# Kernel optimization log

Measured on AMD Instinct MI355X. Metric: run time of the kernel, lower is better.

## Reference

```python
import jax, jax.numpy as jnp
import numpy as np

EPS = 1e-5

def _layernorm(x, g, b):
    m = jnp.mean(x, axis=-1, keepdims=True)
    v = jnp.mean(jnp.square(x - m), axis=-1, keepdims=True)
    return (x - m) * jax.lax.rsqrt(v + EPS) * g + b

def setup_inputs() -> dict:
    key = jax.random.key(0)
    B, S, D, H = 2, 2048, 1024, 16
    F = 4 * D
    ks = jax.random.split(key, 12)
    s = 1.0 / np.sqrt(D)
    inp = {
        "x": jax.random.normal(ks[0], (B, S, D), dtype=jnp.float32),
        "mask": jnp.ones((B, S), dtype=jnp.int32),
        "wq": jax.random.normal(ks[1], (D, D), dtype=jnp.float32) * s,
        "bq": jnp.zeros((D,), jnp.float32),
        "wk": jax.random.normal(ks[2], (D, D), dtype=jnp.float32) * s,
        "bk": jnp.zeros((D,), jnp.float32),
        "wv": jax.random.normal(ks[3], (D, D), dtype=jnp.float32) * s,
        "bv": jnp.zeros((D,), jnp.float32),
        "wo": jax.random.normal(ks[4], (D, D), dtype=jnp.float32) * s,
        "bo": jnp.zeros((D,), jnp.float32),
        "g1": jnp.ones((D,), jnp.float32),
        "be1": jnp.zeros((D,), jnp.float32),
        "g2": jnp.ones((D,), jnp.float32),
        "be2": jnp.zeros((D,), jnp.float32),
        "w1": jax.random.normal(ks[5], (D, F), dtype=jnp.float32) * s,
        "bf1": jnp.zeros((F,), jnp.float32),
        "w2": jax.random.normal(ks[6], (F, D), dtype=jnp.float32) * (1.0 / np.sqrt(F)),
        "bf2": jnp.zeros((D,), jnp.float32),
    }
    return inp

def reference(x, mask, wq, bq, wk, bk, wv, bv, wo, bo, g1, be1, g2, be2, w1, bf1, w2, bf2):
    B, S, D = x.shape
    H = 16
    hd = D // H
    residual = x
    xn = _layernorm(x, g1, be1)
    q = (xn @ wq + bq).reshape(B, S, H, hd).transpose(0, 2, 1, 3)  # [B,H,S,hd]
    k = (xn @ wk + bk).reshape(B, S, H, hd).transpose(0, 2, 1, 3)
    v = (xn @ wv + bv).reshape(B, S, H, hd).transpose(0, 2, 1, 3)
    scores = jnp.einsum('bhqd,bhkd->bhqk', q, k) / np.sqrt(hd)  # [B,H,S,S]
    scores = jnp.where(mask[:, None, None, :] == 0, jnp.float32(-1e9), scores)
    attn = jax.nn.softmax(scores, axis=-1)
    attended = jnp.einsum('bhqk,bhkd->bhqd', attn, v)
    attended = attended.transpose(0, 2, 1, 3).reshape(B, S, D)
    x = residual + (attended @ wo + bo)
    residual = x
    xn = _layernorm(x, g2, be2)
    ff = jax.nn.relu(xn @ w1 + bf1) @ w2 + bf2
    return residual + ff
```

## Files before the change

kernel.cpp:

```cpp
#include <hip/hip_runtime.h>
#include <hip/hip_bf16.h>


using bf16 = __hip_bfloat16;
typedef short bf16x8 __attribute__((ext_vector_type(8)));
typedef short bf16x4v __attribute__((ext_vector_type(4)));
typedef float f32x4 __attribute__((ext_vector_type(4)));

#if defined(__has_builtin)
#  if __has_builtin(__builtin_amdgcn_mfma_f32_16x16x16bf16_1k)
#    define HAVE_MFMA_K16 1
#  endif
#endif

__device__ __forceinline__ float toF(float v) { return v; }
__device__ __forceinline__ float toF(bf16 v) { return __bfloat162float(v); }
__device__ __forceinline__ void storeF(float* p, float v) { *p = v; }
__device__ __forceinline__ void storeF(bf16* p, float v) { *p = __float2bfloat16(v); }

__device__ __forceinline__ float waveReduceSum(float v) {
    #pragma unroll
    for (int o = 32; o > 0; o >>= 1) v += __shfl_down(v, o, 64);
    return v;
}

__device__ __forceinline__ void async16(const bf16* g, bf16* l) {
    __builtin_amdgcn_global_load_lds(
        (const __attribute__((address_space(1))) unsigned int*)g,
        (__attribute__((address_space(3))) unsigned int*)l,
        16, 0, 0);
}

__device__ __forceinline__ unsigned short bf16bits(float x) {
    union { bf16 h; unsigned short u; } e; e.h = __float2bfloat16(x);
    return e.u;
}

__global__ __launch_bounds__(256) void transpose_all(
        const float* __restrict__ wq, const float* __restrict__ wk,
        const float* __restrict__ wv, const float* __restrict__ wo,
        const float* __restrict__ w1, const float* __restrict__ w2,
        bf16* __restrict__ wqkvT, bf16* __restrict__ woT,
        bf16* __restrict__ w1T, bf16* __restrict__ w2T) {
    __shared__ float t[32][33];
    const int tI = blockIdx.x;
    const float* in; bf16* outT; int R, C, tl;
    if (tI < 4096) {
        const int seg = tI >> 10; tl = tI & 1023; R = 1024; C = 1024;
        in = (seg == 0) ? wq : (seg == 1) ? wk : (seg == 2) ? wv : wo;
        outT = (seg == 3) ? woT : wqkvT + (size_t)seg * 1024 * 1024;
    } else if (tI < 8192) {
        tl = tI - 4096; in = w1; outT = w1T; R = 1024; C = 4096;
    } else {
        tl = tI - 8192; in = w2; outT = w2T; R = 4096; C = 1024;
    }
    const int tc = C >> 5;
    const int c0 = (tl % tc) * 32, r0 = (tl / tc) * 32;
    const int lx = threadIdx.x & 31, ly = threadIdx.x >> 5;
    #pragma unroll
    for (int i = 0; i < 32; i += 8)
        t[ly + i][lx] = in[(size_t)(r0 + ly + i) * C + c0 + lx];
    __syncthreads();
    #pragma unroll
    for (int i = 0; i < 32; i += 8)
        outT[(size_t)(c0 + ly + i) * R + r0 + lx] = __float2bfloat16(t[lx][ly + i]);
}

template <typename InT>
__global__ __launch_bounds__(256) void ln_kernel(const InT* __restrict__ x,
                                                 const float* __restrict__ g,
                                                 const float* __restrict__ b,
                                                 bf16* __restrict__ out, int D) {
    const int row = blockIdx.x;
    const InT* xr = x + (size_t)row * D;
    float s = 0.f, s2 = 0.f;
    for (int i = threadIdx.x; i < D; i += 256) {
        float v = toF(xr[i]);
        s += v; s2 += v * v;
    }
    __shared__ float ws[4], ws2[4];
    int lane = threadIdx.x & 63, wid = threadIdx.x >> 6;
    s = waveReduceSum(s); s2 = waveReduceSum(s2);
    if (lane == 0) { ws[wid] = s; ws2[wid] = s2; }
    __syncthreads();
    float ts = ws[0] + ws[1] + ws[2] + ws[3];
    float ts2 = ws2[0] + ws2[1] + ws2[2] + ws2[3];
    float mean = ts / D;
    float var = ts2 / D - mean * mean;
    float rstd = rsqrtf(var + 1e-5f);
    bf16* outr = out + (size_t)row * D;
    for (int i = threadIdx.x; i < D; i += 256) {
        float v = (toF(xr[i]) - mean) * rstd * g[i] + b[i];
        outr[i] = __float2bfloat16(v);
    }
}

template <int BM, typename OutT, typename ResidT, bool RELU, bool HAS_RESID, bool BIAS3>
__global__ __launch_bounds__(256) void gemm_mfma(const bf16* __restrict__ A,
                                                 const bf16* __restrict__ BT,
                                                 const float* __restrict__ bias,
                                                 const float* __restrict__ biasK,
                                                 const float* __restrict__ biasV,
                                                 const ResidT* __restrict__ resid,
                                                 OutT* __restrict__ C,
                                                 int M, int N, int K) {
    constexpr int BK = 32;
    constexpr int MI = BM / 32;
    __shared__ bf16 As[BM][BK];
    __shared__ bf16 Bs[128][BK];
    const int tid = threadIdx.x, lane = tid & 63, wid = tid >> 6;
    const int m0 = blockIdx.y * BM, n0 = blockIdx.x * 128;
    const int wm = (BM == 128) ? (wid >> 1) * 64 : (wid & 1) * 32;
    const int wn = (BM == 128) ? (wid & 1) * 64 : (wid >> 1) * 64;

    f32x4 acc[MI][4] = {};

    const int srow = wid * 16 + (lane >> 2);
    const int scol = (lane & 3) * 8;
    const size_t aBase0 = (size_t)(m0 + srow) * K + scol;
    const size_t aBase1 = (size_t)(m0 + (BM == 128 ? 64 : 0) + srow) * K + scol;
    const size_t bBase0 = (size_t)(n0 + srow) * K + scol;
    const size_t bBase1 = (size_t)(n0 + 64 + srow) * K + scol;

    const int fr = lane & 15;
    const int fk = (lane >> 4) * 8;

    for (int k0 = 0; k0 < K; k0 += BK) {
        async16(A + aBase0 + k0, &As[wid * 16][0]);
        if (BM == 128)
            async16(A + aBase1 + k0, &As[(BM == 128 ? 64 : 0) + wid * 16][0]);
        async16(BT + bBase0 + k0, &Bs[wid * 16][0]);
        async16(BT + bBase1 + k0, &Bs[64 + wid * 16][0]);
        __syncthreads();

        bf16x8 aF[MI], bF[4];
        #pragma unroll
        for (int i = 0; i < MI; ++i)
            aF[i] = *(const bf16x8*)&As[wm + i * 16 + fr][fk];
        #pragma unroll
        for (int j = 0; j < 4; ++j)
            bF[j] = *(const bf16x8*)&Bs[wn + j * 16 + fr][fk];
        #pragma unroll
        for (int i = 0; i < MI; ++i)
            #pragma unroll
            for (int j = 0; j < 4; ++j)
                acc[i][j] = __builtin_amdgcn_mfma_f32_16x16x32_bf16(
                    aF[i], bF[j], acc[i][j], 0, 0, 0);
        __syncthreads();
    }

    const int col_l = lane & 15, row_l = (lane >> 4) * 4;
    #pragma unroll
    for (int j = 0; j < 4; ++j) {
        const int col = n0 + wn + j * 16 + col_l;
        float bvv;
        if (BIAS3) {
            const float* bp = (col < 1024) ? bias : ((col < 2048) ? biasK : biasV);
            bvv = bp[col & 1023];
        } else {
            bvv = bias[col];
        }
        #pragma unroll
        for (int i = 0; i < MI; ++i) {
            #pragma unroll
            for (int r = 0; r < 4; ++r) {
                const int row = m0 + wm + i * 16 + row_l + r;
                float v = acc[i][j][r] + bvv;
                if (RELU) v = fmaxf(v, 0.f);
                if (HAS_RESID) v += toF(resid[(size_t)row * N + col]);
                storeF(&C[(size_t)row * N + col], v);
            }
        }
    }
}

#if HAVE_MFMA_K16
__global__ __launch_bounds__(256) void attn_mfma(const bf16* __restrict__ qkv,
                                                 const int* __restrict__ mask,
                                                 bf16* __restrict__ outp,
                                                 int B, int S, int LD) {
    const int q0 = blockIdx.x * 128;
    const int h = blockIdx.y, b = blockIdx.z;
    const int Do = 1024;
    const int tid = threadIdx.x, lane = tid & 63, wid = tid >> 6;
    const int n = lane & 15, kg = lane >> 4;

    __shared__ bf16 Ks[64][66];
    __shared__ bf16 Vt[64][68];
    __shared__ float Mskf[64];

    bf16x8 qf[2][2];
    #pragma unroll
    for (int u = 0; u < 2; ++u) {
        const bf16* qp = qkv + ((size_t)(b * S + q0 + wid * 32 + u * 16 + n)) * LD + h * 64 + kg * 8;
        union { uint4 uu; bf16x8 v; unsigned short s[8]; } c[2];
        c[0].uu = *(const uint4*)qp;
        c[1].uu = *(const uint4*)(qp + 32);
        #pragma unroll
        for (int t = 0; t < 2; ++t) {
            #pragma unroll
            for (int i = 0; i < 8; ++i) {
                union { float f; unsigned int u2; } d;
                d.u2 = ((unsigned int)c[t].s[i]) << 16;
                c[t].s[i] = bf16bits(d.f * 0.125f);
            }
            qf[u][t] = c[t].v;
        }
    }

    f32x4 acc[2][4] = {};
    float m[2] = {-1e30f, -1e30f}, l[2] = {0.f, 0.f};

    const int sr = tid >> 2, sc = (tid & 3) * 16;
    const int jp = tid & 31, dg = (tid >> 5) * 8;
    const bf16* kbase = qkv + (size_t)(b * S) * LD + 1024 + h * 64;
    const bf16* vbase = qkv + (size_t)(b * S) * LD + 2048 + h * 64;

    for (int j0 = 0; j0 < S; j0 += 64) {
        __syncthreads();
        {
            const bf16* kp = kbase + (size_t)(j0 + sr) * LD + sc;
            uint4 ka = *(const uint4*)kp;
            uint4 kc = *(const uint4*)(kp + 8);
            uint* kd = (uint*)((char*)&Ks[0][0] + sr * 132 + sc * 2);
            kd[0] = ka.x; kd[1] = ka.y; kd[2] = ka.z; kd[3] = ka.w;
            kd[4] = kc.x; kd[5] = kc.y; kd[6] = kc.z; kd[7] = kc.w;

            const bf16* vp = vbase + (size_t)(j0 + 2 * jp) * LD + dg;
            union { uint4 u; unsigned short s[8]; } va, vc;
            va.u = *(const uint4*)vp;
            vc.u = *(const uint4*)(vp + LD);
            #pragma unroll
            for (int i = 0; i < 8; ++i) {
                unsigned int pk = (unsigned int)va.s[i] | ((unsigned int)vc.s[i] << 16);
                *(unsigned int*)((char*)&Vt[0][0] + (size_t)(dg + i) * 136 + jp * 4) = pk;
            }
            if (tid < 64) Mskf[tid] = (mask[b * S + j0 + tid] == 0) ? -1e9f : 0.f;
        }
        __syncthreads();

        f32x4 st[2][4] = {};
        #pragma unroll
        for (int ks = 0; ks < 2; ++ks) {
            #pragma unroll
            for (int jt = 0; jt < 4; ++jt) {
                union { uint u[4]; bf16x8 v; } kf;
                const uint* bp = (const uint*)((const char*)&Ks[0][0]
                                 + (size_t)(jt * 16 + n) * 132 + ks * 64 + kg * 16);
                kf.u[0] = bp[0]; kf.u[1] = bp[1]; kf.u[2] = bp[2]; kf.u[3] = bp[3];
                st[0][jt] = __builtin_amdgcn_mfma_f32_16x16x32_bf16(kf.v, qf[0][ks], st[0][jt], 0, 0, 0);
                st[1][jt] = __builtin_amdgcn_mfma_f32_16x16x32_bf16(kf.v, qf[1][ks], st[1][jt], 0, 0, 0);
            }
        }

        bf16x4v pf[2][4];
        #pragma unroll
        for (int u = 0; u < 2; ++u) {
            float mx = m[u];
            #pragma unroll
            for (int jt = 0; jt < 4; ++jt) {
                f32x4 mb = *(const f32x4*)&Mskf[jt * 16 + kg * 4];
                #pragma unroll
                for (int r = 0; r < 4; ++r) {
                    st[u][jt][r] += mb[r];
                    mx = fmaxf(mx, st[u][jt][r]);
                }
            }
            mx = fmaxf(mx, __shfl_xor(mx, 16, 64));
            mx = fmaxf(mx, __shfl_xor(mx, 32, 64));
            float alpha = __expf(m[u] - mx);
            m[u] = mx;
            float ls = 0.f;
            #pragma unroll
            for (int jt = 0; jt < 4; ++jt) {
                union { unsigned short s[4]; bf16x4v v; } pk;
                #pragma unroll
                for (int r = 0; r < 4; ++r) {
                    float p = __expf(st[u][jt][r] - mx);
                    ls += p;
                    pk.s[r] = bf16bits(p);
                }
                pf[u][jt] = pk.v;
            }
            ls += __shfl_xor(ls, 16, 64);
            ls += __shfl_xor(ls, 32, 64);
            l[u] = l[u] * alpha + ls;
            #pragma unroll
            for (int dt = 0; dt < 4; ++dt)
                #pragma unroll
                for (int r = 0; r < 4; ++r) acc[u][dt][r] *= alpha;
        }

        #pragma unroll
        for (int jt = 0; jt < 4; ++jt) {
            #pragma unroll
            for (int dt = 0; dt < 4; ++dt) {
                union { uint u[2]; bf16x4v v; } vf;
                const uint* vpp = (const uint*)((const char*)&Vt[0][0]
                                  + (size_t)(dt * 16 + n) * 136 + jt * 32 + kg * 8);
                vf.u[0] = vpp[0]; vf.u[1] = vpp[1];
                acc[0][dt] = __builtin_amdgcn_mfma_f32_16x16x16bf16_1k(vf.v, pf[0][jt], acc[0][dt], 0, 0, 0);
                acc[1][dt] = __builtin_amdgcn_mfma_f32_16x16x16bf16_1k(vf.v, pf[1][jt], acc[1][dt], 0, 0, 0);
            }
        }
    }

    #pragma unroll
    for (int u = 0; u < 2; ++u) {
        float inv = (l[u] > 0.f) ? (1.f / l[u]) : 0.f;
        bf16* op = outp + ((size_t)(b * S + q0 + wid * 32 + u * 16 + n)) * Do + h * 64;
        #pragma unroll
        for (int dt = 0; dt < 4; ++dt) {
            union { unsigned short s[4]; uint2 u2; } w;
            #pragma unroll
            for (int r = 0; r < 4; ++r) w.s[r] = bf16bits(acc[u][dt][r] * inv);
            *(uint2*)(op + dt * 16 + kg * 4) = w.u2;
        }
    }
}
#else
__global__ __launch_bounds__(256) void attn_mfma(const bf16* __restrict__ qkv,
                                                 const int* __restrict__ mask,
                                                 bf16* __restrict__ outp,
                                                 int B, int S, int LD) {
    const int h = blockIdx.y, b = blockIdx.z;
    const int Do = 1024;
    const int tid = threadIdx.x, lane = tid & 63, wid = tid >> 6;
    const int n = lane & 15, kg = lane >> 4;

    __shared__ bf16 Ks[64][66];
    __shared__ bf16 Vt[64][66];
    __shared__ bf16 Plds[4][16][66];
    __shared__ int  Msk[64];

    for (int half = 0; half < 2; ++half) {
        const int q0 = blockIdx.x * 128 + half * 64;
        __syncthreads();

        bf16x8 qf[2];
        {
            const bf16* qp = qkv + ((size_t)(b * S + q0 + wid * 16 + n)) * LD + h * 64 + kg * 8;
            union { uint4 u; bf16x8 v; } c0, c1;
            c0.u = *(const uint4*)qp;
            c1.u = *(const uint4*)(qp + 32);
            qf[0] = c0.v; qf[1] = c1.v;
        }

        f32x4 acc_o[4] = {};
        float m_r[4] = {-1e30f, -1e30f, -1e30f, -1e30f};
        float l_r[4] = {0.f, 0.f, 0.f, 0.f};

        const int sr = tid >> 2;
        const int sc = (tid & 3) * 16;
        const bf16* kbase = qkv + (size_t)(b * S) * LD + 1024 + h * 64;
        const bf16* vbase = qkv + (size_t)(b * S) * LD + 2048 + h * 64;

        for (int j0 = 0; j0 < S; j0 += 64) {
            __syncthreads();
            {
                const bf16* kp = kbase + (size_t)(j0 + sr) * LD + sc;
                uint4 ka = *(const uint4*)kp;
                uint4 kbv = *(const uint4*)(kp + 8);
                uint* kd = (uint*)((char*)&Ks[0][0] + sr * 132 + sc * 2);
                kd[0] = ka.x; kd[1] = ka.y; kd[2] = ka.z; kd[3] = ka.w;
                kd[4] = kbv.x; kd[5] = kbv.y; kd[6] = kbv.z; kd[7] = kbv.w;

                const bf16* vp = vbase + (size_t)(j0 + sr) * LD + sc;
                union { uint4 u[2]; unsigned short s[16]; } vv;
                vv.u[0] = *(const uint4*)vp;
                vv.u[1] = *(const uint4*)(vp + 8);
                #pragma unroll
                for (int i = 0; i < 16; ++i)
                    *((unsigned short*)((char*)&Vt[0][0] + (size_t)(sc + i) * 132 + sr * 2)) = vv.s[i];

                if (tid < 64) Msk[tid] = mask[b * S + j0 + tid];
            }
            __syncthreads();

            f32x4 st[4] = {};
            #pragma unroll
            for (int ks = 0; ks < 2; ++ks) {
                #pragma unroll
                for (int jt = 0; jt < 4; ++jt) {
                    union { uint u[4]; bf16x8 v; } bf;
                    const uint* bp = (const uint*)((const char*)&Ks[0][0]
                                     + (size_t)(jt * 16 + n) * 132 + ks * 64 + kg * 16);
                    bf.u[0] = bp[0]; bf.u[1] = bp[1]; bf.u[2] = bp[2]; bf.u[3] = bp[3];
                    st[jt] = __builtin_amdgcn_mfma_f32_16x16x32_bf16(qf[ks], bf.v, st[jt], 0, 0, 0);
                }
            }

            int mk[4];
            #pragma unroll
            for (int jt = 0; jt < 4; ++jt) mk[jt] = Msk[jt * 16 + n];

            #pragma unroll
            for (int r = 0; r < 4; ++r) {
                float mx = -1e30f;
                #pragma unroll
                for (int jt = 0; jt < 4; ++jt) {
                    float s = st[jt][r] * 0.125f;
                    if (mk[jt] == 0) s = -1e9f;
                    st[jt][r] = s;
                    mx = fmaxf(mx, s);
                }
                #pragma unroll
                for (int o = 1; o < 16; o <<= 1) mx = fmaxf(mx, __shfl_xor(mx, o, 64));
                float newm = fmaxf(m_r[r], mx);
                float alpha = __expf(m_r[r] - newm);
                m_r[r] = newm;
                float ls = 0.f;
                #pragma unroll
                for (int jt = 0; jt < 4; ++jt) {
                    float p = __expf(st[jt][r] - newm);
                    ls += p;
                    Plds[wid][kg * 4 + r][jt * 16 + n] = __float2bfloat16(p);
                }
                #pragma unroll
                for (int o = 1; o < 16; o <<= 1) ls += __shfl_xor(ls, o, 64);
                l_r[r] = l_r[r] * alpha + ls;
                #pragma unroll
                for (int dt = 0; dt < 4; ++dt) acc_o[dt][r] *= alpha;
            }

            __asm__ volatile("s_waitcnt lgkmcnt(0)" ::: "memory");

            #pragma unroll
            for (int ks = 0; ks < 2; ++ks) {
                union { uint u[4]; bf16x8 v; } af;
                const uint* ap = (const uint*)((const char*)&Plds[wid][0][0]
                                 + (size_t)n * 132 + ks * 64 + kg * 16);
                af.u[0] = ap[0]; af.u[1] = ap[1]; af.u[2] = ap[2]; af.u[3] = ap[3];
                #pragma unroll
                for (int dt = 0; dt < 4; ++dt) {
                    union { uint u[4]; bf16x8 v; } bf;
                    const uint* bp = (const uint*)((const char*)&Vt[0][0]
                                     + (size_t)(dt * 16 + n) * 132 + ks * 64 + kg * 16);
                    bf.u[0] = bp[0]; bf.u[1] = bp[1]; bf.u[2] = bp[2]; bf.u[3] = bp[3];
                    acc_o[dt] = __builtin_amdgcn_mfma_f32_16x16x32_bf16(af.v, bf.v, acc_o[dt], 0, 0, 0);
                }
            }
        }

        #pragma unroll
        for (int r = 0; r < 4; ++r) {
            float inv = (l_r[r] > 0.f) ? (1.f / l_r[r]) : 0.f;
            bf16* op = outp + ((size_t)(b * S + q0 + wid * 16 + kg * 4 + r)) * Do + h * 64 + n;
            #pragma unroll
            for (int dt = 0; dt < 4; ++dt)
                op[dt * 16] = __float2bfloat16(acc_o[dt][r] * inv);
        }
    }
}
#endif

extern "C" void kernel_launch(void* const* d_in, const int* in_sizes, int n_in,
                              void* d_out, int out_size, void* d_ws, size_t ws_size,
                              hipStream_t stream) {
    const int B = 2, S = 2048, D = 1024, H = 16, F = 4096;
    const int M = B * S;

    const float* x   = (const float*)d_in[0];
    const int*   mask= (const int*)  d_in[1];
    const float* wq  = (const float*)d_in[2];
    const float* bq  = (const float*)d_in[3];
    const float* wk  = (const float*)d_in[4];
    const float* bk  = (const float*)d_in[5];
    const float* wv  = (const float*)d_in[6];
    const float* bv  = (const float*)d_in[7];
    const float* wo  = (const float*)d_in[8];
    const float* bo  = (const float*)d_in[9];
    const float* g1  = (const float*)d_in[10];
    const float* be1 = (const float*)d_in[11];
    const float* g2  = (const float*)d_in[12];
    const float* be2 = (const float*)d_in[13];
    const float* w1  = (const float*)d_in[14];
    const float* bf1 = (const float*)d_in[15];
    const float* w2  = (const float*)d_in[16];
    const float* bf2 = (const float*)d_in[17];
    float* out = (float*)d_out;

    char* ws = (char*)d_ws;
    const size_t MB = 1024 * 1024;
    bf16* wqkvT = (bf16*)(ws + 0 * MB);
    bf16* woT   = (bf16*)(ws + 6 * MB);
    bf16* w1T   = (bf16*)(ws + 8 * MB);
    bf16* w2T   = (bf16*)(ws + 16 * MB);
    bf16* xn    = (bf16*)(ws + 24 * MB);
    bf16* qkv   = (bf16*)(ws + 32 * MB);
    bf16* att   = xn;

    const bool fullM = (ws_size >= 64 * MB);

    transpose_all<<<12288, 256, 0, stream>>>(wq, wk, wv, wo, w1, w2,
                                             wqkvT, woT, w1T, w2T);

    ln_kernel<float><<<M, 256, 0, stream>>>(x, g1, be1, xn, D);

    gemm_mfma<128, bf16, float, false, false, true><<<dim3(3072 / 128, M / 128), 256, 0, stream>>>(
        xn, wqkvT, bq, bk, bv, (const float*)nullptr, qkv, M, 3072, D);

    attn_mfma<<<dim3(S / 128, H, B), 256, 0, stream>>>(qkv, mask, att, B, S, 3072);

    gemm_mfma<64, float, float, false, true, false><<<dim3(D / 128, M / 64), 256, 0, stream>>>(
        att, woT, bo, nullptr, nullptr, x, out, M, D, D);

    if (fullM) {
        bf16* hid = (bf16*)(ws + 24 * MB);
        bf16* xn2 = (bf16*)(ws + 56 * MB);
        ln_kernel<float><<<M, 256, 0, stream>>>(out, g2, be2, xn2, D);
        gemm_mfma<128, bf16, float, true, false, false><<<dim3(F / 128, M / 128), 256, 0, stream>>>(
            xn2, w1T, bf1, nullptr, nullptr, (const float*)nullptr, hid, M, F, D);
        gemm_mfma<64, float, float, false, true, false><<<dim3(D / 128, M / 64), 256, 0, stream>>>(
            hid, w2T, bf2, nullptr, nullptr, out, out, M, D, F);
    } else {
        bf16* xn2 = (bf16*)(ws + 32 * MB);
        bf16* hid = (bf16*)(ws + 40 * MB);
        const int CH = 2048;
        ln_kernel<float><<<M, 256, 0, stream>>>(out, g2, be2, xn2, D);
        for (int c = 0; c < M / CH; ++c) {
            const size_t roff = (size_t)c * CH;
            gemm_mfma<128, bf16, float, true, false, false><<<dim3(F / 128, CH / 128), 256, 0, stream>>>(
                xn2 + roff * D, w1T, bf1, nullptr, nullptr, (const float*)nullptr, hid, CH, F, D);
            gemm_mfma<64, float, float, false, true, false><<<dim3(D / 128, CH / 64), 256, 0, stream>>>(
                hid, w2T, bf2, nullptr, nullptr, out + roff * D, out + roff * D, CH, D, F);
        }
    }
}
```

Baseline: 429.9 us.

## Double GEMM K-tile with XOR-swizzled LDS and use exp2 softmax in attention

The GEMM now loads a 64-wide K slice per iteration, so there are half as many barriers. It stores tiles in LDS with an XOR swizzle on 16-byte chunks to avoid bank conflicts, and each iteration runs two MFMA sub-steps. In attention, log2(e) is folded into the Q scale so exp2f can replace __expf. The probabilities are truncated to bf16 before they are summed, which keeps the row sum consistent with the PV operands and replaces rounding with a mask. These changes raise LDS usage per block and slightly change numerics (truncation instead of round-to-nearest).

```diff
diff --git a/kernel.cpp b/kernel.cpp
--- a/kernel.cpp
+++ b/kernel.cpp
@@ -104,8 +104,10 @@
                                                  const ResidT* __restrict__ resid,
                                                  OutT* __restrict__ C,
                                                  int M, int N, int K) {
-    constexpr int BK = 32;
+    constexpr int BK = 64;
     constexpr int MI = BM / 32;
+    constexpr int AROWS = BM / 4;
+    constexpr int ASEC = AROWS / 8;
     __shared__ bf16 As[BM][BK];
     __shared__ bf16 Bs[128][BK];
     const int tid = threadIdx.x, lane = tid & 63, wid = tid >> 6;
@@ -115,37 +117,42 @@
 
     f32x4 acc[MI][4] = {};
 
-    const int srow = wid * 16 + (lane >> 2);
-    const int scol = (lane & 3) * 8;
-    const size_t aBase0 = (size_t)(m0 + srow) * K + scol;
-    const size_t aBase1 = (size_t)(m0 + (BM == 128 ? 64 : 0) + srow) * K + scol;
-    const size_t bBase0 = (size_t)(n0 + srow) * K + scol;
-    const size_t bBase1 = (size_t)(n0 + 64 + srow) * K + scol;
+    const int srow = lane >> 3;
+    const int scol = ((lane & 7) ^ srow) * 8;
+    const bf16* Abase = A + (size_t)(m0 + wid * AROWS + srow) * K + scol;
+    const bf16* Bbase = BT + (size_t)(n0 + wid * 32 + srow) * K + scol;
 
     const int fr = lane & 15;
-    const int fk = (lane >> 4) * 8;
+    const int kg = lane >> 4;
 
     for (int k0 = 0; k0 < K; k0 += BK) {
-        async16(A + aBase0 + k0, &As[wid * 16][0]);
-        if (BM == 128)
-            async16(A + aBase1 + k0, &As[(BM == 128 ? 64 : 0) + wid * 16][0]);
-        async16(BT + bBase0 + k0, &Bs[wid * 16][0]);
-        async16(BT + bBase1 + k0, &Bs[64 + wid * 16][0]);
+        #pragma unroll
+        for (int s = 0; s < ASEC; ++s)
+            async16(Abase + (size_t)(s * 8) * K + k0, &As[wid * AROWS + s * 8][0]);
+        #pragma unroll
+        for (int s = 0; s < 4; ++s)
+            async16(Bbase + (size_t)(s * 8) * K + k0, &Bs[wid * 32 + s * 8][0]);
         __syncthreads();
 
-        bf16x8 aF[MI], bF[4];
-        #pragma unroll
-        for (int i = 0; i < MI; ++i)
-            aF[i] = *(const bf16x8*)&As[wm + i * 16 + fr][fk];
-        #pragma unroll
-        for (int j = 0; j < 4; ++j)
-            bF[j] = *(const bf16x8*)&Bs[wn + j * 16 + fr][fk];
-        #pragma unroll
-        for (int i = 0; i < MI; ++i)
+        #pragma unroll
+        for (int ks = 0; ks < 2; ++ks) {
+            const int pc = ((ks * 4 + kg) ^ (fr & 7)) * 16;
+            bf16x8 aF[MI], bF[4];
+            #pragma unroll
+            for (int i = 0; i < MI; ++i)
+                aF[i] = *(const bf16x8*)((const char*)&As[0][0]
+                         + (size_t)(wm + i * 16 + fr) * 128 + pc);
             #pragma unroll
             for (int j = 0; j < 4; ++j)
-                acc[i][j] = __builtin_amdgcn_mfma_f32_16x16x32_bf16(
-                    aF[i], bF[j], acc[i][j], 0, 0, 0);
+                bF[j] = *(const bf16x8*)((const char*)&Bs[0][0]
+                         + (size_t)(wn + j * 16 + fr) * 128 + pc);
+            #pragma unroll
+            for (int i = 0; i < MI; ++i)
+                #pragma unroll
+                for (int j = 0; j < 4; ++j)
+                    acc[i][j] = __builtin_amdgcn_mfma_f32_16x16x32_bf16(
+                        aF[i], bF[j], acc[i][j], 0, 0, 0);
+        }
         __syncthreads();
     }
 
@@ -189,6 +196,7 @@
     __shared__ bf16 Vt[64][68];
     __shared__ float Mskf[64];
 
+    const float QSCALE = 0.125f * 1.4426950408889634f;
     bf16x8 qf[2][2];
     #pragma unroll
     for (int u = 0; u < 2; ++u) {
@@ -202,7 +210,7 @@
             for (int i = 0; i < 8; ++i) {
                 union { float f; unsigned int u2; } d;
                 d.u2 = ((unsigned int)c[t].s[i]) << 16;
-                c[t].s[i] = bf16bits(d.f * 0.125f);
+                c[t].s[i] = bf16bits(d.f * QSCALE);
             }
             qf[u][t] = c[t].v;
         }
@@ -268,7 +276,7 @@
             }
             mx = fmaxf(mx, __shfl_xor(mx, 16, 64));
             mx = fmaxf(mx, __shfl_xor(mx, 32, 64));
-            float alpha = __expf(m[u] - mx);
+            float alpha = exp2f(m[u] - mx);
             m[u] = mx;
             float ls = 0.f;
             #pragma unroll
@@ -276,9 +284,11 @@
                 union { unsigned short s[4]; bf16x4v v; } pk;
                 #pragma unroll
                 for (int r = 0; r < 4; ++r) {
-                    float p = __expf(st[u][jt][r] - mx);
-                    ls += p;
-                    pk.s[r] = bf16bits(p);
+                    union { float f; unsigned int u2; } p;
+                    p.f = exp2f(st[u][jt][r] - mx);
+                    p.u2 &= 0xffff0000u;
+                    ls += p.f;
+                    pk.s[r] = (unsigned short)(p.u2 >> 16);
                 }
                 pf[u][jt] = pk.v;
             }
```

Measured after the change: 414.1 us. -3.7%, faster.
